# Performance work log

Hardware: AMD Instinct MI355X
Metric: run time of the kernel (lower is better)

The kernel has to match this reference:

```python
import jax, jax.numpy as jnp
import numpy as np
import math

SENTINEL = 1.0e6  # eta/phi value assigned to inactive (pt<=0) objects
BIG = 1.0e6       # dR placeholder for non-lower-triangular entries


def _remove_duplicates(objs, threshold):
    """objs: (B, n, 3) with columns (pt, eta, phi). Zeros out objects that
    are within dR < threshold of a later object in the group (faithful to
    the TF strictly-lower-triangular / reduce over rows logic)."""
    n = objs.shape[1]
    active = objs[..., 0] > 0.0                              # (B, n)
    eta = jnp.where(active, objs[..., 1], SENTINEL)
    phi = jnp.where(active, objs[..., 2], SENTINEL)
    deta = eta[:, :, None] - eta[:, None, :]                 # (B, n, n)
    dphi = jnp.mod(phi[:, :, None] - phi[:, None, :] + math.pi,
                   2.0 * math.pi) - math.pi
    dr2 = deta * deta + dphi * dphi
    # strictly lower triangular mask (row i > col j), same as
    # logical_not(band_part(ones, 0, -1)) in TF
    tri = jnp.tril(jnp.ones((n, n), dtype=bool), k=-1)       # (n, n)
    # safe sqrt: only evaluate where the mask keeps the value
    dr = jnp.sqrt(jnp.where(tri, dr2, 1.0))
    replaced = jnp.where(tri, dr, BIG)                       # (B, n, n)
    # TF reduce_any(..., axis=0) per event -> axis=1 of batched tensor
    duplicates = jnp.any(replaced < threshold, axis=1)       # (B, n)
    return jnp.where(duplicates[..., None], 0.0, objs)


def duplicate_removal(x, threshold):
    jets = _remove_duplicates(x[:, 0:6], threshold)
    electrons = _remove_duplicates(x[:, 6:9], threshold)
    muons = _remove_duplicates(x[:, 9:12], threshold)
    photons = _remove_duplicates(x[:, 12:15], threshold)
    met = x[:, 15:16]
    return jnp.concatenate([jets, electrons, muons, photons, met], axis=1)


def setup_inputs() -> dict:
    key = jax.random.key(0)
    x = jax.random.normal(key, (1000000, 16, 3), dtype=jnp.float32)
    return {"x": x}


def reference(x):
    return duplicate_removal(x, 0.05)
```

## Files before the change

### kernel.cpp

```cpp
#include <hip/hip_runtime.h>
#include <math.h>

#define PI_F    3.14159274101257324e0f
#define TWOPI_F 6.28318548202514648e0f
#define SENT_F  1000000.0f

template <int OFF, int N>
__device__ __forceinline__ unsigned group_dup(const float* r) {
    float e[N], p[N];
#pragma unroll
    for (int k = 0; k < N; ++k) {
        float pt = r[3 * (OFF + k) + 0];
        bool act = pt > 0.0f;
        e[k] = act ? r[3 * (OFF + k) + 1] : SENT_F;
        p[k] = act ? r[3 * (OFF + k) + 2] : SENT_F;
    }
    unsigned dup = 0;
#pragma unroll
    for (int j = 0; j < N - 1; ++j) {
        bool d = false;
#pragma unroll
        for (int i = j + 1; i < N; ++i) {
            float deta = e[i] - e[j];
            float dd   = (p[i] - p[j]) + PI_F;
            float m    = fmodf(dd, TWOPI_F);
            m = (m < 0.0f) ? (m + TWOPI_F) : m;
            float dphi = m - PI_F;
            float dr2 = __fadd_rn(__fmul_rn(deta, deta), __fmul_rn(dphi, dphi));
            float dr  = __fsqrt_rn(dr2);
            d = d || (dr < 0.05f);
        }
        if (d) dup |= (1u << (OFF + j));
    }
    return dup;
}

__global__ __launch_bounds__(256) void dup_removal_kernel(
    const float4* __restrict__ in, float4* __restrict__ out, int B) {
    __shared__ float rowbuf[256 * 48];
    __shared__ unsigned maskbuf[256];

    const int t = threadIdx.x;
    const long long base4  = (long long)blockIdx.x * 3072;
    const long long total4 = (long long)B * 12;

    float4 v[12];
#pragma unroll
    for (int i = 0; i < 12; ++i) {
        long long g = base4 + t + 256 * i;
        if (g < total4) {
            v[i] = in[g];
            ((float4*)rowbuf)[t + 256 * i] = v[i];
        }
    }
    __syncthreads();

    const int row = blockIdx.x * 256 + t;
    unsigned dup = 0;
    if (row < B) {
        const float* r = rowbuf + t * 48;
        dup  = group_dup<0, 6>(r);
        dup |= group_dup<6, 3>(r);
        dup |= group_dup<9, 3>(r);
        dup |= group_dup<12, 3>(r);
    }
    maskbuf[t] = dup;
    __syncthreads();

#pragma unroll
    for (int i = 0; i < 12; ++i) {
        long long g = base4 + t + 256 * i;
        if (g < total4) {
            int local = t + 256 * i;
            int rl = local / 12;
            int f  = local - rl * 12;
            unsigned m = maskbuf[rl];
            int k0 = 4 * f;
            float4 w = v[i];
            if ((m >> ((k0 + 0) / 3)) & 1u) w.x = 0.0f;
            if ((m >> ((k0 + 1) / 3)) & 1u) w.y = 0.0f;
            if ((m >> ((k0 + 2) / 3)) & 1u) w.z = 0.0f;
            if ((m >> ((k0 + 3) / 3)) & 1u) w.w = 0.0f;
            out[g] = w;
        }
    }
}

extern "C" void kernel_launch(void* const* d_in, const int* in_sizes, int n_in,
                              void* d_out, int out_size, void* d_ws, size_t ws_size,
                              hipStream_t stream) {
    const float4* x = (const float4*)d_in[0];
    float4* out = (float4*)d_out;
    int B = in_sizes[0] / 48;
    int grid = (B + 255) / 256;
    dup_removal_kernel<<<grid, 256, 0, stream>>>(x, out, B);
}
```

Baseline: 349.2 us.

## Halve rows per block, pad shared rows, replace fmodf with double trunc-FMA

Each 256-thread block now stages 128 rows into a padded shared buffer (stride 49) to cut LDS bank conflicts, and only half the threads do the pairwise work. fmodf is replaced by a double-precision trunc/FMA reduction, and inactive objects are handled with explicit flags instead of sentinel values. The per-row mask is expanded to a per-float 64-bit mask so the store phase applies it with a nibble lookup. Launch bounds are raised for occupancy. The costs are idle threads during compute and double-precision math, which may be slow or subtly differ from fmodf.

```diff
diff --git a/kernel.cpp b/kernel.cpp
--- a/kernel.cpp
+++ b/kernel.cpp
@@ -1,86 +1,106 @@
 #include <hip/hip_runtime.h>
 #include <math.h>
 
-#define PI_F    3.14159274101257324e0f
-#define TWOPI_F 6.28318548202514648e0f
-#define SENT_F  1000000.0f
+#define PI_F        3.14159274101257324e0f
+#define TWOPI_F     6.28318548202514648e0f
+#define TWOPI_D     ((double)TWOPI_F)
+#define INV_TWOPI_D (1.0 / (double)TWOPI_F)
+
+#define ROWS_PER_BLOCK 128
+#define ROW_STRIDE     49
+
+__device__ __forceinline__ int pair_close(float ei, float ej, float pi_, float pj) {
+    float deta = __fsub_rn(ei, ej);
+    float dd   = __fadd_rn(__fsub_rn(pi_, pj), PI_F);
+    double ddd = (double)dd;
+    double q   = trunc(ddd * INV_TWOPI_D);
+    float  m   = (float)fma(-q, TWOPI_D, ddd);
+    if (m < 0.0f) m = __fadd_rn(m, TWOPI_F);
+    float dphi = __fsub_rn(m, PI_F);
+    float dr2  = __fadd_rn(__fmul_rn(deta, deta), __fmul_rn(dphi, dphi));
+    return __fsqrt_rn(dr2) < 0.05f;
+}
 
 template <int OFF, int N>
 __device__ __forceinline__ unsigned group_dup(const float* r) {
     float e[N], p[N];
+    int   a[N];
 #pragma unroll
     for (int k = 0; k < N; ++k) {
         float pt = r[3 * (OFF + k) + 0];
-        bool act = pt > 0.0f;
-        e[k] = act ? r[3 * (OFF + k) + 1] : SENT_F;
-        p[k] = act ? r[3 * (OFF + k) + 2] : SENT_F;
+        a[k] = pt > 0.0f;
+        e[k] = r[3 * (OFF + k) + 1];
+        p[k] = r[3 * (OFF + k) + 2];
     }
     unsigned dup = 0;
 #pragma unroll
     for (int j = 0; j < N - 1; ++j) {
-        bool d = false;
+        int d = 0;
 #pragma unroll
         for (int i = j + 1; i < N; ++i) {
-            float deta = e[i] - e[j];
-            float dd   = (p[i] - p[j]) + PI_F;
-            float m    = fmodf(dd, TWOPI_F);
-            m = (m < 0.0f) ? (m + TWOPI_F) : m;
-            float dphi = m - PI_F;
-            float dr2 = __fadd_rn(__fmul_rn(deta, deta), __fmul_rn(dphi, dphi));
-            float dr  = __fsqrt_rn(dr2);
-            d = d || (dr < 0.05f);
+            int close = pair_close(e[i], e[j], p[i], p[j]);
+            d |= (a[i] & a[j] & close) | ((a[i] | a[j]) ^ 1);
         }
         if (d) dup |= (1u << (OFF + j));
     }
     return dup;
 }
 
-__global__ __launch_bounds__(256) void dup_removal_kernel(
+__global__ __launch_bounds__(256, 6) void dup_removal_kernel(
     const float4* __restrict__ in, float4* __restrict__ out, int B) {
-    __shared__ float rowbuf[256 * 48];
-    __shared__ unsigned maskbuf[256];
+    __shared__ float rowbuf[ROWS_PER_BLOCK * ROW_STRIDE];
+    __shared__ unsigned long long maskbuf[ROWS_PER_BLOCK];
 
     const int t = threadIdx.x;
-    const long long base4  = (long long)blockIdx.x * 3072;
+    const long long base4  = (long long)blockIdx.x * (ROWS_PER_BLOCK * 12);
     const long long total4 = (long long)B * 12;
 
-    float4 v[12];
+    float4 v[6];
 #pragma unroll
-    for (int i = 0; i < 12; ++i) {
+    for (int i = 0; i < 6; ++i) {
         long long g = base4 + t + 256 * i;
         if (g < total4) {
             v[i] = in[g];
-            ((float4*)rowbuf)[t + 256 * i] = v[i];
+            int local = t + 256 * i;
+            int rl = local / 12;
+            int f  = local - rl * 12;
+            float* dstp = &rowbuf[rl * ROW_STRIDE + 4 * f];
+            dstp[0] = v[i].x; dstp[1] = v[i].y; dstp[2] = v[i].z; dstp[3] = v[i].w;
         }
     }
     __syncthreads();
 
-    const int row = blockIdx.x * 256 + t;
-    unsigned dup = 0;
-    if (row < B) {
-        const float* r = rowbuf + t * 48;
-        dup  = group_dup<0, 6>(r);
-        dup |= group_dup<6, 3>(r);
-        dup |= group_dup<9, 3>(r);
-        dup |= group_dup<12, 3>(r);
+    if (t < ROWS_PER_BLOCK) {
+        int row = blockIdx.x * ROWS_PER_BLOCK + t;
+        unsigned dup = 0;
+        if (row < B) {
+            const float* r = rowbuf + t * ROW_STRIDE;
+            dup  = group_dup<0, 6>(r);
+            dup |= group_dup<6, 3>(r);
+            dup |= group_dup<9, 3>(r);
+            dup |= group_dup<12, 3>(r);
+        }
+        unsigned long long fm = 0ull;
+#pragma unroll
+        for (int o = 0; o < 15; ++o)
+            fm |= (unsigned long long)((dup >> o) & 1u) * (7ull << (3 * o));
+        maskbuf[t] = fm;
     }
-    maskbuf[t] = dup;
     __syncthreads();
 
 #pragma unroll
-    for (int i = 0; i < 12; ++i) {
+    for (int i = 0; i < 6; ++i) {
         long long g = base4 + t + 256 * i;
         if (g < total4) {
             int local = t + 256 * i;
             int rl = local / 12;
             int f  = local - rl * 12;
-            unsigned m = maskbuf[rl];
-            int k0 = 4 * f;
+            unsigned nib = (unsigned)(maskbuf[rl] >> (4 * f)) & 0xFu;
             float4 w = v[i];
-            if ((m >> ((k0 + 0) / 3)) & 1u) w.x = 0.0f;
-            if ((m >> ((k0 + 1) / 3)) & 1u) w.y = 0.0f;
-            if ((m >> ((k0 + 2) / 3)) & 1u) w.z = 0.0f;
-            if ((m >> ((k0 + 3) / 3)) & 1u) w.w = 0.0f;
+            if (nib & 1u) w.x = 0.0f;
+            if (nib & 2u) w.y = 0.0f;
+            if (nib & 4u) w.z = 0.0f;
+            if (nib & 8u) w.w = 0.0f;
             out[g] = w;
         }
     }
@@ -92,6 +112,6 @@
     const float4* x = (const float4*)d_in[0];
     float4* out = (float4*)d_out;
     int B = in_sizes[0] / 48;
-    int grid = (B + 255) / 256;
+    int grid = (B + ROWS_PER_BLOCK - 1) / ROWS_PER_BLOCK;
     dup_removal_kernel<<<grid, 256, 0, stream>>>(x, out, B);
 }
```

Result: faster. 323.5 us (-7.4%).
